# Performance work log

Hardware: AMD Instinct MI355X
Metric: run time of the kernel (lower is better)

The kernel has to match this reference:

```python
import jax, jax.numpy as jnp
import numpy as np

B, C, H, W = 8, 192, 120, 120
WSIZES = [4, 8, 12]
BN_EPS = 1e-5


def _conv1x1(t, w, b):
    # t: [b,c,h,w], w: [o,c], b: [o]
    return jnp.einsum('oc,bchw->bohw', w, t) + b[None, :, None, None]


def _bn(t, g, bb, m, v):
    scale = (g * jax.lax.rsqrt(v + BN_EPS))[None, :, None, None]
    return (t - m[None, :, None, None]) * scale + bb[None, :, None, None]


def _partition_qv(t, ws):
    # t: [b, 2c, h, w] -> qx, vx each [b*nh*nw, ws*ws, c]
    b, c2, h, w = t.shape
    c = c2 // 2
    nh, nw = h // ws, w // ws
    t = t.reshape(b, 2, c, nh, ws, nw, ws)
    t = t.transpose(1, 0, 3, 5, 4, 6, 2).reshape(2, b * nh * nw, ws * ws, c)
    return t[0], t[1]


def _merge(t, ws, b, h, w):
    # t: [b*nh*nw, ws*ws, c] -> [b, c, h, w]
    nh, nw = h // ws, w // ws
    c = t.shape[-1]
    t = t.reshape(b, nh, nw, ws, ws, c)
    return t.transpose(0, 5, 1, 3, 2, 4).reshape(b, c, h, w)


def setup_inputs() -> dict:
    key = jax.random.key(0)
    ks = jax.random.split(key, 6)
    d = {}
    d['x'] = jax.random.normal(ks[0], (B, C, H, W), jnp.float32)
    d['y'] = jax.random.normal(ks[1], (B, C, H, W), jnp.float32)
    d['w_in'] = jax.random.normal(ks[2], (2 * C, C), jnp.float32) * 0.05
    d['b_in'] = jax.random.normal(ks[3], (2 * C,), jnp.float32) * 0.01
    d['bn_gamma'] = jnp.ones((2 * C,), jnp.float32)
    d['bn_beta'] = jnp.zeros((2 * C,), jnp.float32)
    d['bn_mean'] = jnp.zeros((2 * C,), jnp.float32)
    d['bn_var'] = jnp.ones((2 * C,), jnp.float32)
    d['w_out'] = jax.random.normal(ks[4], (C, C), jnp.float32) * 0.05
    d['b_out'] = jax.random.normal(ks[5], (C,), jnp.float32) * 0.01
    return d


def reference(x, y, w_in, b_in, bn_gamma, bn_beta, bn_mean, bn_var, w_out, b_out):
    b, c, h, w = x.shape
    xp = _bn(_conv1x1(x, w_in, b_in), bn_gamma, bn_beta, bn_mean, bn_var)
    yp = _bn(_conv1x1(y, w_in, b_in), bn_gamma, bn_beta, bn_mean, bn_var)
    chunk = c * 2 // 3
    y1s, atns = [], []
    for i, ws in enumerate(WSIZES):
        x_ = xp[:, i * chunk:(i + 1) * chunk]
        y_ = yp[:, i * chunk:(i + 1) * chunk]
        s = ws // 2  # shifts > 0 -> shifted windows
        x_ = jnp.roll(x_, (-s, -s), axis=(2, 3))
        y_ = jnp.roll(y_, (-s, -s), axis=(2, 3))
        qx, vx = _partition_qv(x_, ws)
        qy, vy = _partition_qv(y_, ws)
        atn = jax.nn.softmax(jnp.einsum('nqc,nkc->nqk', qx, qy), axis=-1)
        o = jnp.einsum('nqk,nkc->nqc', atn, vx)
        o = _merge(o, ws, b, h, w)
        o = jnp.roll(o, (s, s), axis=(2, 3))
        y1s.append(o)
        atns.append(atn)
    y1 = _conv1x1(jnp.concatenate(y1s, axis=1), w_out, b_out)
    return (y1, atns[0], atns[1], atns[2])
```

## Files before the change

kernel.cpp:

```cpp
#include <hip/hip_runtime.h>

typedef __bf16 bf16x8 __attribute__((ext_vector_type(8)));
typedef float f32x4 __attribute__((ext_vector_type(4)));
typedef unsigned int u32x4 __attribute__((ext_vector_type(4)));
typedef unsigned int u32x2 __attribute__((ext_vector_type(2)));

#define HW 14400
#define CIN 192

__device__ __forceinline__ unsigned short f2bf(float f) {
  unsigned int u = __builtin_bit_cast(unsigned int, f);
  u = (u + 0x7FFFu + ((u >> 16) & 1u)) >> 16;
  return (unsigned short)u;
}
__device__ __forceinline__ float bf2f(unsigned short h) {
  unsigned int u = ((unsigned int)h) << 16;
  return __builtin_bit_cast(float, u);
}

__global__ void prep_kernel(const float* __restrict__ w_in, const float* __restrict__ b_in,
                            const float* __restrict__ g, const float* __restrict__ be,
                            const float* __restrict__ mu, const float* __restrict__ va,
                            const float* __restrict__ w_out,
                            unsigned short* __restrict__ wx, unsigned short* __restrict__ wy,
                            unsigned short* __restrict__ wo,
                            float* __restrict__ bx, float* __restrict__ by) {
  int idx = blockIdx.x * 256 + threadIdx.x;
  if (idx < 384 * 192) {
    int o = idx / 192;
    float s = g[o] * rsqrtf(va[o] + 1e-5f);
    wx[idx] = f2bf(w_in[idx] * s);
  } else if (idx < 384 * 192 + 192 * 192) {
    int j = idx - 384 * 192;
    int jo = j / 192, c = j % 192;
    int o = (jo >> 6) * 128 + (jo & 63);
    float s = g[o] * rsqrtf(va[o] + 1e-5f);
    wy[j] = f2bf(w_in[o * 192 + c] * s);
  } else if (idx < 384 * 192 + 2 * 192 * 192) {
    int j = idx - (384 * 192 + 192 * 192);
    wo[j] = f2bf(w_out[j]);
  }
  if (idx < 384) {
    float s = g[idx] * rsqrtf(va[idx] + 1e-5f);
    bx[idx] = (b_in[idx] - mu[idx]) * s + be[idx];
  } else if (idx < 384 + 192) {
    int jo = idx - 384;
    int o = (jo >> 6) * 128 + (jo & 63);
    float s = g[o] * rsqrtf(va[o] + 1e-5f);
    by[jo] = (b_in[o] - mu[o]) * s + be[o];
  }
}

template <int NOUT>
__launch_bounds__(256, 2)
__global__ void conv_in_kernel(const float* __restrict__ X,
                               const unsigned short* __restrict__ Wb,
                               const float* __restrict__ bias,
                               unsigned short* __restrict__ Out) {
  constexpr int NT = NOUT / 64;
  __shared__ unsigned short a_lds[64 * 40];
  __shared__ unsigned short b_lds[NOUT * 40];
  const int t = threadIdx.x;
  const int wave = t >> 6, lane = t & 63;
  const int l15 = lane & 15, l4 = lane >> 4;
  const int b = blockIdx.x / 225;
  const int px0 = (blockIdx.x % 225) * 64;
  const float* Xb = X + (size_t)b * CIN * HW + px0;
  const int wo0 = wave * (NOUT / 4);

  f32x4 acc[4][NT];
#pragma unroll
  for (int n = 0; n < NT; ++n) {
    float bv = bias[wo0 + n * 16 + l15];
    f32x4 iv = {bv, bv, bv, bv};
#pragma unroll
    for (int m = 0; m < 4; ++m) acc[m][n] = iv;
  }

  for (int kc = 0; kc < 6; ++kc) {
    const int c0 = kc * 32;
#pragma unroll
    for (int p = 0; p < 2; ++p) {
      int idx = p * 256 + t;
      int c = idx >> 4, px4 = (idx & 15) * 4;
      f32x4 v = *reinterpret_cast<const f32x4*>(Xb + (size_t)(c0 + c) * HW + px4);
      a_lds[(px4 + 0) * 40 + c] = f2bf(v[0]);
      a_lds[(px4 + 1) * 40 + c] = f2bf(v[1]);
      a_lds[(px4 + 2) * 40 + c] = f2bf(v[2]);
      a_lds[(px4 + 3) * 40 + c] = f2bf(v[3]);
    }
#pragma unroll
    for (int p = 0; p < NOUT / 64; ++p) {
      int o = p * 64 + (t >> 2), c8 = (t & 3) * 8;
      *reinterpret_cast<u32x4*>(&b_lds[o * 40 + c8]) =
          *reinterpret_cast<const u32x4*>(Wb + (size_t)o * CIN + c0 + c8);
    }
    __syncthreads();
    bf16x8 af[4];
#pragma unroll
    for (int m = 0; m < 4; ++m)
      af[m] = *reinterpret_cast<const bf16x8*>(&a_lds[(m * 16 + l15) * 40 + l4 * 8]);
#pragma unroll
    for (int n = 0; n < NT; ++n) {
      bf16x8 bfr = *reinterpret_cast<const bf16x8*>(&b_lds[(wo0 + n * 16 + l15) * 40 + l4 * 8]);
#pragma unroll
      for (int m = 0; m < 4; ++m)
        acc[m][n] = __builtin_amdgcn_mfma_f32_16x16x32_bf16(af[m], bfr, acc[m][n], 0, 0, 0);
    }
    __syncthreads();
  }

  unsigned short* Ob = Out + ((size_t)b * HW + px0) * NOUT;
#pragma unroll
  for (int m = 0; m < 4; ++m) {
#pragma unroll
    for (int r = 0; r < 4; ++r) {
      int px = m * 16 + l4 * 4 + r;
      unsigned short* dst = Ob + (size_t)px * NOUT + wo0 + l15;
#pragma unroll
      for (int n = 0; n < NT; ++n) dst[n * 16] = f2bf(acc[m][n][r]);
    }
  }
}

template <int WS, int SI, int NTHR>
__launch_bounds__(NTHR, 2)
__global__ void attn_kernel(const unsigned short* __restrict__ XP,
                            const unsigned short* __restrict__ YQ,
                            unsigned short* __restrict__ Z,
                            float* __restrict__ ATN) {
  constexpr int S = WS / 2, L = WS * WS, NH = 120 / WS, TT = L / 16;
  constexpr int NWAVE = NTHR / 64;
  constexpr int SMAX = (TT + NWAVE - 1) / NWAVE;
  constexpr int KP = ((L + 31) / 32) * 32;
  constexpr int PL = KP + 8;
  constexpr int KSTEPS = KP / 32;
  constexpr int POOLE = (L * 72 > L * PL) ? L * 72 : L * PL;
  __shared__ unsigned short pool[POOLE];
  __shared__ unsigned short vt_lds[64 * PL];
  unsigned short* k_lds = pool;
  unsigned short* p_lds = pool;

  const int t = threadIdx.x;
  const int win = blockIdx.x;
  const int b = win / (NH * NH);
  const int r_ = win % (NH * NH);
  const int ih = r_ / NH, iw = r_ % NH;
  const int wave = t >> 6, lane = t & 63, l15 = lane & 15, l4 = lane >> 4;

  auto pixof = [&](int e) {
    int p = e / WS, qc = e % WS;
    int h = ih * WS + p + S; if (h >= 120) h -= 120;
    int w = iw * WS + qc + S; if (w >= 120) w -= 120;
    return b * HW + h * 120 + w;
  };

  for (int idx = t; idx < L * 8; idx += NTHR) {
    int e = idx >> 3, c8 = (idx & 7) * 8;
    *reinterpret_cast<u32x4*>(&k_lds[e * 72 + c8]) =
        *reinterpret_cast<const u32x4*>(YQ + (size_t)pixof(e) * 192 + SI * 64 + c8);
  }
  for (int idx = t; idx < L * 8; idx += NTHR) {
    int e = idx >> 3, c8 = (idx & 7) * 8;
    u32x4 v = *reinterpret_cast<const u32x4*>(XP + (size_t)pixof(e) * 384 + SI * 128 + 64 + c8);
    const unsigned short* vh = reinterpret_cast<const unsigned short*>(&v);
#pragma unroll
    for (int j = 0; j < 8; ++j) vt_lds[(c8 + j) * PL + e] = vh[j];
  }
  if constexpr (KP > L) {
    for (int idx = t; idx < 64 * (KP - L); idx += NTHR)
      vt_lds[(idx / (KP - L)) * PL + L + (idx % (KP - L))] = 0;
  }

  bf16x8 af[SMAX][2];
#pragma unroll
  for (int si = 0; si < SMAX; ++si) {
    int ti = wave + si * NWAVE;
    if (ti < TT) {
      const unsigned short* qp =
          XP + (size_t)pixof(ti * 16 + l15) * 384 + SI * 128 + l4 * 8;
      af[si][0] = *reinterpret_cast<const bf16x8*>(qp);
      af[si][1] = *reinterpret_cast<const bf16x8*>(qp + 32);
    }
  }
  __syncthreads();

  f32x4 sacc[SMAX][TT];
#pragma unroll
  for (int si = 0; si < SMAX; ++si)
#pragma unroll
    for (int tj = 0; tj < TT; ++tj) sacc[si][tj] = f32x4{0.f, 0.f, 0.f, 0.f};
#pragma unroll
  for (int tj = 0; tj < TT; ++tj) {
    bf16x8 b0 = *reinterpret_cast<const bf16x8*>(&k_lds[(tj * 16 + l15) * 72 + l4 * 8]);
    bf16x8 b1 = *reinterpret_cast<const bf16x8*>(&k_lds[(tj * 16 + l15) * 72 + 32 + l4 * 8]);
#pragma unroll
    for (int si = 0; si < SMAX; ++si) {
      int ti = wave + si * NWAVE;
      if (ti < TT) {
        sacc[si][tj] = __builtin_amdgcn_mfma_f32_16x16x32_bf16(af[si][0], b0, sacc[si][tj], 0, 0, 0);
        sacc[si][tj] = __builtin_amdgcn_mfma_f32_16x16x32_bf16(af[si][1], b1, sacc[si][tj], 0, 0, 0);
      }
    }
  }

  float inv_[SMAX][4];
#pragma unroll
  for (int si = 0; si < SMAX; ++si) {
    int ti = wave + si * NWAVE;
    if (ti < TT) {
#pragma unroll
      for (int r = 0; r < 4; ++r) {
        float m = -1e30f;
#pragma unroll
        for (int tj = 0; tj < TT; ++tj) m = fmaxf(m, sacc[si][tj][r]);
#pragma unroll
        for (int mk = 1; mk < 16; mk <<= 1) m = fmaxf(m, __shfl_xor(m, mk, 64));
        float s = 0.f;
#pragma unroll
        for (int tj = 0; tj < TT; ++tj) {
          float e = __expf(sacc[si][tj][r] - m);
          sacc[si][tj][r] = e;
          s += e;
        }
#pragma unroll
        for (int mk = 1; mk < 16; mk <<= 1) s += __shfl_xor(s, mk, 64);
        inv_[si][r] = 1.f / s;
      }
    }
  }

  __syncthreads();

  if constexpr (KP > L) {
#pragma unroll
    for (int si = 0; si < SMAX; ++si) {
      int ti = wave + si * NWAVE;
      if (ti < TT)
        *reinterpret_cast<unsigned long long*>(
            &p_lds[(ti * 16 + l15) * PL + L + l4 * 4]) = 0ULL;
    }
  }

  float* aout = ATN + (size_t)win * L * L;
#pragma unroll
  for (int si = 0; si < SMAX; ++si) {
    int ti = wave + si * NWAVE;
    if (ti < TT) {
#pragma unroll
      for (int tj = 0; tj < TT; ++tj)
#pragma unroll
        for (int r = 0; r < 4; ++r) {
          float p = sacc[si][tj][r] * inv_[si][r];
          int row = ti * 16 + l4 * 4 + r, col = tj * 16 + l15;
          aout[row * L + col] = p;
          p_lds[row * PL + col] = f2bf(p);
        }
    }
  }
  __syncthreads();

#pragma unroll
  for (int si = 0; si < SMAX; ++si) {
    int ti = wave + si * NWAVE;
    if (ti < TT) {
      bf16x8 ap[KSTEPS];
#pragma unroll
      for (int kk = 0; kk < KSTEPS; ++kk)
        ap[kk] = *reinterpret_cast<const bf16x8*>(&p_lds[(ti * 16 + l15) * PL + kk * 32 + l4 * 8]);
      int opix[4];
#pragma unroll
      for (int r = 0; r < 4; ++r) opix[r] = pixof(ti * 16 + l4 * 4 + r);
#pragma unroll
      for (int cj = 0; cj < 4; ++cj) {
        f32x4 o = {0.f, 0.f, 0.f, 0.f};
#pragma unroll
        for (int kk = 0; kk < KSTEPS; ++kk) {
          bf16x8 bv = *reinterpret_cast<const bf16x8*>(&vt_lds[(cj * 16 + l15) * PL + kk * 32 + l4 * 8]);
          o = __builtin_amdgcn_mfma_f32_16x16x32_bf16(ap[kk], bv, o, 0, 0, 0);
        }
#pragma unroll
        for (int r = 0; r < 4; ++r)
          Z[(size_t)opix[r] * 192 + SI * 64 + cj * 16 + l15] = f2bf(o[r]);
      }
    }
  }
}

__launch_bounds__(256, 2)
__global__ void conv_out_kernel(const unsigned short* __restrict__ Z,
                                const unsigned short* __restrict__ Wo,
                                const float* __restrict__ bout,
                                float* __restrict__ Y1) {
  __shared__ unsigned short z_lds[64 * 40];
  __shared__ unsigned short w_lds[192 * 40];
  const int t = threadIdx.x, wave = t >> 6, lane = t & 63;
  const int l15 = lane & 15, l4 = lane >> 4;
  const int b = blockIdx.x / 225, px0 = (blockIdx.x % 225) * 64;
  const unsigned short* Zb = Z + ((size_t)b * HW + px0) * 192;
  const int wo0 = wave * 48;
  f32x4 acc[3][4];
#pragma unroll
  for (int m = 0; m < 3; ++m) {
    f32x4 bv;
#pragma unroll
    for (int r = 0; r < 4; ++r) bv[r] = bout[wo0 + m * 16 + l4 * 4 + r];
#pragma unroll
    for (int n = 0; n < 4; ++n) acc[m][n] = bv;
  }
  for (int kc = 0; kc < 6; ++kc) {
    const int c0 = kc * 32;
    {
      int px = t >> 2, c8 = (t & 3) * 8;
      *reinterpret_cast<u32x4*>(&z_lds[px * 40 + c8]) =
          *reinterpret_cast<const u32x4*>(Zb + (size_t)px * 192 + c0 + c8);
    }
#pragma unroll
    for (int p = 0; p < 3; ++p) {
      int o = p * 64 + (t >> 2), c8 = (t & 3) * 8;
      *reinterpret_cast<u32x4*>(&w_lds[o * 40 + c8]) =
          *reinterpret_cast<const u32x4*>(Wo + (size_t)o * 192 + c0 + c8);
    }
    __syncthreads();
    bf16x8 bfr[4];
#pragma unroll
    for (int n = 0; n < 4; ++n)
      bfr[n] = *reinterpret_cast<const bf16x8*>(&z_lds[(n * 16 + l15) * 40 + l4 * 8]);
#pragma unroll
    for (int m = 0; m < 3; ++m) {
      bf16x8 af = *reinterpret_cast<const bf16x8*>(&w_lds[(wo0 + m * 16 + l15) * 40 + l4 * 8]);
#pragma unroll
      for (int n = 0; n < 4; ++n)
        acc[m][n] = __builtin_amdgcn_mfma_f32_16x16x32_bf16(af, bfr[n], acc[m][n], 0, 0, 0);
    }
    __syncthreads();
  }
  float* Yb = Y1 + (size_t)b * 192 * HW + px0;
#pragma unroll
  for (int m = 0; m < 3; ++m) {
#pragma unroll
    for (int r = 0; r < 4; ++r) {
      int o = wo0 + m * 16 + l4 * 4 + r;
      float* dst = Yb + (size_t)o * HW + l15;
#pragma unroll
      for (int n = 0; n < 4; ++n) dst[n * 16] = acc[m][n][r];
    }
  }
}

extern "C" void kernel_launch(void* const* d_in, const int* in_sizes, int n_in,
                              void* d_out, int out_size, void* d_ws, size_t ws_size,
                              hipStream_t stream) {
  const float* x = (const float*)d_in[0];
  const float* y = (const float*)d_in[1];
  const float* w_in = (const float*)d_in[2];
  const float* b_in = (const float*)d_in[3];
  const float* g = (const float*)d_in[4];
  const float* be = (const float*)d_in[5];
  const float* mu = (const float*)d_in[6];
  const float* va = (const float*)d_in[7];
  const float* w_out = (const float*)d_in[8];
  const float* b_out = (const float*)d_in[9];
  char* ws = (char*)d_ws;
  unsigned short* wx = (unsigned short*)(ws + 0);
  unsigned short* wy = (unsigned short*)(ws + 147456);
  unsigned short* wo = (unsigned short*)(ws + 221184);
  float* bx = (float*)(ws + 294912);
  float* by = (float*)(ws + 296448);
  unsigned short* xp = (unsigned short*)(ws + 297216);
  unsigned short* yq = (unsigned short*)(ws + 297216 + (size_t)115200 * 384 * 2);
  unsigned short* z  = (unsigned short*)(ws + 297216 + (size_t)115200 * 384 * 2 +
                                         (size_t)115200 * 192 * 2);
  float* out = (float*)d_out;

  prep_kernel<<<576, 256, 0, stream>>>(w_in, b_in, g, be, mu, va, w_out, wx, wy, wo, bx, by);
  conv_in_kernel<384><<<1800, 256, 0, stream>>>(x, wx, bx, xp);
  conv_in_kernel<192><<<1800, 256, 0, stream>>>(y, wy, by, yq);
  attn_kernel<4, 0, 64><<<7200, 64, 0, stream>>>(xp, yq, z, out + 22118400);
  attn_kernel<8, 1, 256><<<1800, 256, 0, stream>>>(xp, yq, z, out + 23961600);
  attn_kernel<12, 2, 256><<<800, 256, 0, stream>>>(xp, yq, z, out + 31334400);
  conv_out_kernel<<<1800, 256, 0, stream>>>(z, wo, b_out, out);
}
```

Baseline: 225.5 us.

## Widen conv_in to six waves and pack bf16 output stores via channel permutation

```diff
diff --git a/kernel.cpp b/kernel.cpp
--- a/kernel.cpp
+++ b/kernel.cpp
@@ -38,7 +38,10 @@
     wy[j] = f2bf(w_in[o * 192 + c] * s);
   } else if (idx < 384 * 192 + 2 * 192 * 192) {
     int j = idx - (384 * 192 + 192 * 192);
-    wo[j] = f2bf(w_out[j]);
+    int o = j / 192, cs = j % 192;
+    int s = cs & 63;
+    int src = (cs & ~63) | ((s & 3) * 16 + (s >> 2));
+    wo[j] = f2bf(w_out[o * 192 + src]);
   }
   if (idx < 384) {
     float s = g[idx] * rsqrtf(va[idx] + 1e-5f);
@@ -52,36 +55,36 @@
 }
 
 template <int NOUT>
-__launch_bounds__(256, 2)
+__launch_bounds__(384, 2)
 __global__ void conv_in_kernel(const float* __restrict__ X,
                                const unsigned short* __restrict__ Wb,
                                const float* __restrict__ bias,
                                unsigned short* __restrict__ Out) {
-  constexpr int NT = NOUT / 64;
+  constexpr int M = (NOUT == 384) ? 4 : 2;
+  constexpr int WCH = (NOUT == 384) ? 4 : 2;
   __shared__ unsigned short a_lds[64 * 40];
   __shared__ unsigned short b_lds[NOUT * 40];
   const int t = threadIdx.x;
-  const int wave = t >> 6, lane = t & 63;
-  const int l15 = lane & 15, l4 = lane >> 4;
+  const int wave = t >> 6, lane = t & 63, l15 = lane & 15, l4 = lane >> 4;
+  const int wchunk = (NOUT == 384) ? wave : (wave >> 1);
+  const int px_base = (NOUT == 384) ? 0 : ((wave & 1) * 32);
+  const int wo0 = wchunk * 64;
   const int b = blockIdx.x / 225;
   const int px0 = (blockIdx.x % 225) * 64;
   const float* Xb = X + (size_t)b * CIN * HW + px0;
-  const int wo0 = wave * (NOUT / 4);
-
-  f32x4 acc[4][NT];
-#pragma unroll
-  for (int n = 0; n < NT; ++n) {
+
+  f32x4 acc[M][4];
+#pragma unroll
+  for (int n = 0; n < 4; ++n) {
     float bv = bias[wo0 + n * 16 + l15];
-    f32x4 iv = {bv, bv, bv, bv};
-#pragma unroll
-    for (int m = 0; m < 4; ++m) acc[m][n] = iv;
+#pragma unroll
+    for (int m = 0; m < M; ++m) acc[m][n] = f32x4{bv, bv, bv, bv};
   }
 
   for (int kc = 0; kc < 6; ++kc) {
     const int c0 = kc * 32;
-#pragma unroll
-    for (int p = 0; p < 2; ++p) {
-      int idx = p * 256 + t;
+    {
+      int idx = t;
       int c = idx >> 4, px4 = (idx & 15) * 4;
       f32x4 v = *reinterpret_cast<const f32x4*>(Xb + (size_t)(c0 + c) * HW + px4);
       a_lds[(px4 + 0) * 40 + c] = f2bf(v[0]);
@@ -89,36 +92,46 @@
       a_lds[(px4 + 2) * 40 + c] = f2bf(v[2]);
       a_lds[(px4 + 3) * 40 + c] = f2bf(v[3]);
     }
-#pragma unroll
-    for (int p = 0; p < NOUT / 64; ++p) {
-      int o = p * 64 + (t >> 2), c8 = (t & 3) * 8;
+    if (t < 128) {
+      int idx = 384 + t;
+      int c = idx >> 4, px4 = (idx & 15) * 4;
+      f32x4 v = *reinterpret_cast<const f32x4*>(Xb + (size_t)(c0 + c) * HW + px4);
+      a_lds[(px4 + 0) * 40 + c] = f2bf(v[0]);
+      a_lds[(px4 + 1) * 40 + c] = f2bf(v[1]);
+      a_lds[(px4 + 2) * 40 + c] = f2bf(v[2]);
+      a_lds[(px4 + 3) * 40 + c] = f2bf(v[3]);
+    }
+#pragma unroll
+    for (int j = 0; j < WCH; ++j) {
+      int idx = j * 384 + t;
+      int o = idx >> 2, c8 = (idx & 3) * 8;
       *reinterpret_cast<u32x4*>(&b_lds[o * 40 + c8]) =
           *reinterpret_cast<const u32x4*>(Wb + (size_t)o * CIN + c0 + c8);
     }
     __syncthreads();
-    bf16x8 af[4];
-#pragma unroll
-    for (int m = 0; m < 4; ++m)
-      af[m] = *reinterpret_cast<const bf16x8*>(&a_lds[(m * 16 + l15) * 40 + l4 * 8]);
-#pragma unroll
-    for (int n = 0; n < NT; ++n) {
+    bf16x8 af[M];
+#pragma unroll
+    for (int m = 0; m < M; ++m)
+      af[m] = *reinterpret_cast<const bf16x8*>(
+          &a_lds[(px_base + m * 16 + l15) * 40 + l4 * 8]);
+#pragma unroll
+    for (int n = 0; n < 4; ++n) {
       bf16x8 bfr = *reinterpret_cast<const bf16x8*>(&b_lds[(wo0 + n * 16 + l15) * 40 + l4 * 8]);
 #pragma unroll
-      for (int m = 0; m < 4; ++m)
+      for (int m = 0; m < M; ++m)
         acc[m][n] = __builtin_amdgcn_mfma_f32_16x16x32_bf16(af[m], bfr, acc[m][n], 0, 0, 0);
     }
     __syncthreads();
   }
 
-  unsigned short* Ob = Out + ((size_t)b * HW + px0) * NOUT;
-#pragma unroll
-  for (int m = 0; m < 4; ++m) {
+#pragma unroll
+  for (int m = 0; m < M; ++m) {
 #pragma unroll
     for (int r = 0; r < 4; ++r) {
-      int px = m * 16 + l4 * 4 + r;
-      unsigned short* dst = Ob + (size_t)px * NOUT + wo0 + l15;
-#pragma unroll
-      for (int n = 0; n < NT; ++n) dst[n * 16] = f2bf(acc[m][n][r]);
+      int px = px_base + m * 16 + l4 * 4 + r;
+      u32x2 pk = {(unsigned)f2bf(acc[m][0][r]) | ((unsigned)f2bf(acc[m][1][r]) << 16),
+                  (unsigned)f2bf(acc[m][2][r]) | ((unsigned)f2bf(acc[m][3][r]) << 16)};
+      *reinterpret_cast<u32x2*>(Out + ((size_t)b * HW + px0 + px) * NOUT + wo0 + l15 * 4) = pk;
     }
   }
 }
@@ -374,8 +387,8 @@
   float* out = (float*)d_out;
 
   prep_kernel<<<576, 256, 0, stream>>>(w_in, b_in, g, be, mu, va, w_out, wx, wy, wo, bx, by);
-  conv_in_kernel<384><<<1800, 256, 0, stream>>>(x, wx, bx, xp);
-  conv_in_kernel<192><<<1800, 256, 0, stream>>>(y, wy, by, yq);
+  conv_in_kernel<384><<<1800, 384, 0, stream>>>(x, wx, bx, xp);
+  conv_in_kernel<192><<<1800, 384, 0, stream>>>(y, wy, by, yq);
   attn_kernel<4, 0, 64><<<7200, 64, 0, stream>>>(xp, yq, z, out + 22118400);
   attn_kernel<8, 1, 256><<<1800, 256, 0, stream>>>(xp, yq, z, out + 23961600);
   attn_kernel<12, 2, 256><<<800, 256, 0, stream>>>(xp, yq, z, out + 31334400);
```

Measured after the change: 263.2 us. 16.7% more time.
